# Kernel optimization log

Measured on AMD Instinct MI355X. Metric: run time of the kernel, lower is better.

Reference implementation:

```python
import jax, jax.numpy as jnp
import numpy as np

K = 20           # neighbors
ALPHA = 1.0      # clustering alpha
BN_EPS = 1e-5
NEG_SLOPE = 0.2


def knn_idx(x, k):
    # x: (B, C, N) -> idx (B, N, k) of k nearest neighbors by squared L2
    xx = jnp.sum(x * x, axis=1)                      # (B, N)
    inner = jnp.einsum('bcn,bcm->bnm', x, x)         # (B, N, N)
    pd = -xx[:, :, None] + 2.0 * inner - xx[:, None, :]  # negative sq dist
    return jax.lax.top_k(pd, k)[1]


def graph_feature(x, k):
    # x: (B, C, N) -> (B, 2C, N, k): concat(neighbor - center, center)
    xt = jnp.transpose(x, (0, 2, 1))                 # (B, N, C)
    idx = knn_idx(x, k)                              # (B, N, k)
    feat = jax.vmap(lambda f, i: f[i])(xt, idx)      # (B, N, k, C)
    center = jnp.broadcast_to(xt[:, :, None, :], feat.shape)
    out = jnp.concatenate([feat - center, center], axis=-1)
    return jnp.transpose(out, (0, 3, 1, 2))


def batchnorm(x, g, b, axes):
    # training-mode BN: batch statistics over `axes`, channel axis = 1
    m = jnp.mean(x, axes, keepdims=True)
    v = jnp.var(x, axes, keepdims=True)
    shape = [1] * x.ndim
    shape[1] = x.shape[1]
    return (x - m) / jnp.sqrt(v + BN_EPS) * g.reshape(shape) + b.reshape(shape)


def conv_block2d(x, w, g, b):
    # 1x1 Conv2d (no bias) + BN2d + LeakyReLU; x (B,Cin,N,k), w (Cout,Cin)
    y = jnp.einsum('oc,bcnk->bonk', w, x)
    return jax.nn.leaky_relu(batchnorm(y, g, b, (0, 2, 3)), NEG_SLOPE)


def setup_inputs() -> dict:
    key = jax.random.key(0)
    ks = jax.random.split(key, 16)
    B, C, N = 4, 3, 2048
    d = {
        'x1': jax.random.normal(ks[0], (B, C, N), jnp.float32),
        'x2': jax.random.normal(ks[1], (B, C, N), jnp.float32),
        'w1': jax.random.normal(ks[2], (64, 6), jnp.float32) * 0.1,
        'g1': jnp.ones((64,), jnp.float32), 'b1': jnp.zeros((64,), jnp.float32),
        'w2': jax.random.normal(ks[3], (64, 128), jnp.float32) * 0.1,
        'g2': jnp.ones((64,), jnp.float32), 'b2': jnp.zeros((64,), jnp.float32),
        'w3': jax.random.normal(ks[4], (128, 128), jnp.float32) * 0.1,
        'g3': jnp.ones((128,), jnp.float32), 'b3': jnp.zeros((128,), jnp.float32),
        'w4': jax.random.normal(ks[5], (256, 256), jnp.float32) * 0.1,
        'g4': jnp.ones((256,), jnp.float32), 'b4': jnp.zeros((256,), jnp.float32),
        'w5': jax.random.normal(ks[6], (1024, 512), jnp.float32) * 0.05,
        'g5': jnp.ones((1024,), jnp.float32), 'b5': jnp.zeros((1024,), jnp.float32),
        'lw1': jax.random.normal(ks[7], (256, 2048), jnp.float32) * 0.02,
        'lb1': jnp.zeros((256,), jnp.float32),
        'lw2': jax.random.normal(ks[8], (64, 256), jnp.float32) * 0.05,
        'lb2': jnp.zeros((64,), jnp.float32),
        'lw3': jax.random.normal(ks[9], (10, 64), jnp.float32) * 0.1,
        'lb3': jnp.zeros((10,), jnp.float32),
        'cw': jax.random.normal(ks[10], (800, 10), jnp.float32) * 0.1,
    }
    return d


def reference(x1, x2, w1, g1, b1, w2, g2, b2, w3, g3, b3, w4, g4, b4,
              w5, g5, b5, lw1, lb1, lw2, lb2, lw3, lb3, cw):

    def single(x):
        h = conv_block2d(graph_feature(x, K), w1, g1, b1)
        f1 = h.max(axis=-1)                            # (B,64,N)
        h = conv_block2d(graph_feature(f1, K), w2, g2, b2)
        f2 = h.max(axis=-1)                            # (B,64,N)
        h = conv_block2d(graph_feature(f2, K), w3, g3, b3)
        f3 = h.max(axis=-1)                            # (B,128,N)
        h = conv_block2d(graph_feature(f3, K), w4, g4, b4)
        f4 = h.max(axis=-1)                            # (B,256,N)
        h = jnp.concatenate([f1, f2, f3, f4], axis=1)  # (B,512,N)
        h = jnp.einsum('oc,bcn->bon', w5, h)           # 1x1 Conv1d
        h = jax.nn.leaky_relu(batchnorm(h, g5, b5, (0, 2)), NEG_SLOPE)
        z = jnp.concatenate([h.max(axis=-1), h.mean(axis=-1)], axis=1)  # (B,2048)
        z = z @ lw1.T + lb1
        z = z @ lw2.T + lb2
        e = z @ lw3.T + lb3                            # (B,10)
        diff = e[:, None, :] - cw                      # (B,800,10)
        x_dis = jnp.sum(diff * diff, axis=2)           # (B,800)
        q = (1.0 + x_dis / ALPHA) ** (-(ALPHA + 1.0) / 2.0)
        q = q / jnp.sum(q, axis=1, keepdims=True)
        return q, e, x_dis

    q1, e1, xd1 = single(x1)
    q2, e2, xd2 = single(x2)
    d = e1 - e2 + 1e-6  # torch F.pairwise_distance eps
    sim = jnp.sqrt(jnp.sum(d * d, axis=1))
    return (sim, q1, q2, e1, e2, xd1)
```

## Files before the change

kernel.cpp:

```cpp
#include <hip/hip_runtime.h>
#include <math.h>

#define BB 4
#define NN 2048
#define KK 20
#define NEG 0.2f

#define QOFF0 4
#define QOFF1 3204
#define EOFF0 6404
#define EOFF1 6444
#define XDOFF 6484

typedef unsigned short u16;
typedef unsigned int u32;
typedef __attribute__((ext_vector_type(8))) short s16x8;
typedef __attribute__((ext_vector_type(16))) float f32x16;
typedef __attribute__((ext_vector_type(8))) u16 u16x8;

__global__ __launch_bounds__(256) void transpose_x_kernel(
    const float* __restrict__ x, float* __restrict__ fnc, float* __restrict__ xx)
{
    int gid = blockIdx.x * 256 + threadIdx.x;
    int b = gid >> 11, n = gid & 2047;
    float s = 0.f;
#pragma unroll
    for (int c = 0; c < 3; ++c) {
        float v = x[((size_t)b * 3 + c) * NN + n];
        fnc[(size_t)gid * 3 + c] = v;
        s += v * v;
    }
    xx[gid] = s;
}

__global__ __launch_bounds__(256) void norms_kernel(
    const float* __restrict__ h512, int choff, int C, float* __restrict__ xx)
{
    int gid = blockIdx.x * 256 + threadIdx.x;
    const float* p = h512 + (size_t)gid * 512 + choff;
    float s = 0.f;
    for (int c = 0; c < C; ++c) { float v = p[c]; s += v * v; }
    xx[gid] = s;
}

template<int CTRL>
__device__ __forceinline__ float dmax(float v)
{
    int vi = __float_as_int(v);
    int nv = __builtin_amdgcn_update_dpp(vi, vi, CTRL, 0xf, 0xf, false);
    return fmaxf(v, __int_as_float(nv));
}

template<int C>
__global__ __launch_bounds__(512, 4) void knn_kernel(
    const float* __restrict__ fcn,
    const float* __restrict__ fnc,
    int ncs, int choff,
    const float* __restrict__ xx, int* __restrict__ idxout)
{
    __shared__ float sbuf[8][NN];
    int tid = threadIdx.x;
    int bid = blockIdx.x;
    int b   = bid & 3;
    int n0  = (((bid >> 3) << 1) | ((bid >> 2) & 1)) * 8;

    const float* fb = fcn + (size_t)b * C * NN;
    const float* xb = xx + b * NN;
    const float* cbase = fnc + (size_t)(b * NN + n0) * ncs + choff;

    float a0[8], a1[8], a2[8], a3[8];
#pragma unroll
    for (int r = 0; r < 8; ++r) { a0[r] = 0.f; a1[r] = 0.f; a2[r] = 0.f; a3[r] = 0.f; }

    const float* fp = fb + 4 * tid;

    if constexpr (C % 4 == 0) {
        float4 buf[4];
#pragma unroll
        for (int q = 0; q < 4; ++q) buf[q] = *(const float4*)(fp + (size_t)q * NN);
        for (int cg = 0; cg < C; cg += 4) {
            float4 nxt[4];
            if (cg + 4 < C) {
#pragma unroll
                for (int q = 0; q < 4; ++q)
                    nxt[q] = *(const float4*)(fp + (size_t)(cg + 4 + q) * NN);
            } else {
#pragma unroll
                for (int q = 0; q < 4; ++q) nxt[q] = buf[q];
            }
            float4 cv[8];
#pragma unroll
            for (int r = 0; r < 8; ++r)
                cv[r] = *(const float4*)(cbase + (size_t)r * ncs + cg);
#pragma unroll
            for (int r = 0; r < 8; ++r) {
                a0[r] += cv[r].x * buf[0].x; a1[r] += cv[r].x * buf[0].y;
                a2[r] += cv[r].x * buf[0].z; a3[r] += cv[r].x * buf[0].w;
                a0[r] += cv[r].y * buf[1].x; a1[r] += cv[r].y * buf[1].y;
                a2[r] += cv[r].y * buf[1].z; a3[r] += cv[r].y * buf[1].w;
                a0[r] += cv[r].z * buf[2].x; a1[r] += cv[r].z * buf[2].y;
                a2[r] += cv[r].z * buf[2].z; a3[r] += cv[r].z * buf[2].w;
                a0[r] += cv[r].w * buf[3].x; a1[r] += cv[r].w * buf[3].y;
                a2[r] += cv[r].w * buf[3].z; a3[r] += cv[r].w * buf[3].w;
            }
#pragma unroll
            for (int q = 0; q < 4; ++q) buf[q] = nxt[q];
        }
    } else {
        for (int c = 0; c < C; ++c) {
            float cr[8];
#pragma unroll
            for (int r = 0; r < 8; ++r) cr[r] = cbase[(size_t)r * ncs + c];
            float4 v = *(const float4*)(fp + (size_t)c * NN);
#pragma unroll
            for (int r = 0; r < 8; ++r) {
                a0[r] += cr[r] * v.x; a1[r] += cr[r] * v.y;
                a2[r] += cr[r] * v.z; a3[r] += cr[r] * v.w;
            }
        }
    }
    {
        float4 xm = *(const float4*)(xb + 4 * tid);
#pragma unroll
        for (int r = 0; r < 8; ++r) {
            float4 sv = {2.f * a0[r] - xm.x, 2.f * a1[r] - xm.y,
                         2.f * a2[r] - xm.z, 2.f * a3[r] - xm.w};
            *(float4*)&sbuf[r][4 * tid] = sv;
        }
    }
    __syncthreads();

    int w = tid >> 6, lane = tid & 63;
    float* sb = sbuf[w];
    int p = n0 + w;
    int* op = idxout + (size_t)(b * NN + p) * KK;
    const float NINF = -3.4e38f;

    float rv[32];
#pragma unroll
    for (int j = 0; j < 32; ++j) {
        float vv = sb[lane + (j << 6)];
        rv[j] = (lane + (j << 6) == p) ? NINF : vv;
    }
    if (lane == 0) op[0] = p;

    unsigned consumed = 0u;

    float v1 = NINF, v2 = NINF; int j1 = -1, j2 = -1;
#pragma unroll
    for (int j = 0; j < 32; ++j) {
        float vv = rv[j];
        if (vv > v1) { v2 = v1; j2 = j1; v1 = vv; j1 = j; }
        else if (vv > v2) { v2 = vv; j2 = j; }
    }
    int i1 = (j1 < 0) ? -1 : lane + (j1 << 6);
    int i2 = (j2 < 0) ? -1 : lane + (j2 << 6);

    for (int it = 1; it < KK; ++it) {
        float bv = v1;
        bv = dmax<0x111>(bv);
        bv = dmax<0x112>(bv);
        bv = dmax<0x114>(bv);
        bv = dmax<0x118>(bv);
        bv = dmax<0x142>(bv);
        bv = dmax<0x143>(bv);
        float smax = __int_as_float(
            __builtin_amdgcn_readlane(__float_as_int(bv), 63));
        unsigned long long mm = __ballot(v1 == smax);
        int owner = __ffsll(mm) - 1;
        if (lane == owner) {
            op[it] = i1;
            consumed |= 1u << j1;
            v1 = v2; i1 = i2; j1 = j2;
            v2 = NINF; i2 = -1; j2 = -1;
        }
        if (__any(v1 == NINF)) {
            if (v1 == NINF) {
                v1 = NINF; v2 = NINF; j1 = -1; j2 = -1;
#pragma unroll
                for (int j = 0; j < 32; ++j) {
                    if (!(consumed & (1u << j))) {
                        float vv = rv[j];
                        if (vv > v1) { v2 = v1; j2 = j1; v1 = vv; j1 = j; }
                        else if (vv > v2) { v2 = vv; j2 = j; }
                    }
                }
                i1 = (j1 < 0) ? -1 : lane + (j1 << 6);
                i2 = (j2 < 0) ? -1 : lane + (j2 << 6);
            }
        }
    }
}

template<int C, int COUT>
__global__ __launch_bounds__(256) void gemm_gh_kernel(
    const float* __restrict__ fnc, int ncs, int choff,
    const float* __restrict__ W,
    float* __restrict__ G, float* __restrict__ H)
{
    constexpr int GROUPS = 256 / COUT;
    constexpr int RPT = 8 / GROUPS;
    __shared__ float Fs[8][C];
    int tid = threadIdx.x;
    int row0 = blockIdx.x * 8;
    for (int i = tid; i < 8 * C; i += 256) {
        int r = i / C, c = i % C;
        Fs[r][c] = fnc[(size_t)(row0 + r) * ncs + choff + c];
    }
    __syncthreads();
    int o = tid % COUT;
    int r0 = (tid / COUT) * RPT;
    float g[RPT], h[RPT];
#pragma unroll
    for (int r = 0; r < RPT; ++r) { g[r] = 0.f; h[r] = 0.f; }
    const float* wr = W + (size_t)o * 2 * C;
    for (int c = 0; c < C; ++c) {
        float w1 = wr[c], wd = wr[C + c] - w1;
#pragma unroll
        for (int r = 0; r < RPT; ++r) {
            float f = Fs[r0 + r][c];
            g[r] += f * w1; h[r] += f * wd;
        }
    }
#pragma unroll
    for (int r = 0; r < RPT; ++r) {
        size_t rr = (size_t)(row0 + r0 + r) * COUT + o;
        G[rr] = g[r]; H[rr] = h[r];
    }
}

template<int COUT>
__global__ __launch_bounds__(256) void gather_kernel(
    const float* __restrict__ G, const float* __restrict__ H,
    const int* __restrict__ idx,
    float* __restrict__ ymax, float* __restrict__ ymin,
    float* __restrict__ psum, float* __restrict__ psumsq)
{
    constexpr int RPI = 256 / COUT;
    constexpr int NITER = 16 / RPI;
    int tid = threadIdx.x;
    int o = tid % COUT;
    int rsub = tid / COUT;
    int row0 = blockIdx.x * 16;
    float s = 0.f, s2 = 0.f;
    for (int it = 0; it < NITER; ++it) {
        int r = row0 + it * RPI + rsub;
        int b = r >> 11;
        float h = H[(size_t)r * COUT + o];
        const int* ip = idx + (size_t)r * KK;
        float mx = -3.4e38f, mn = 3.4e38f;
#pragma unroll
        for (int j = 0; j < KK; ++j) {
            int m = ip[j];
            float g = G[((size_t)(b << 11) + m) * COUT + o];
            float y = g + h;
            mx = fmaxf(mx, y); mn = fminf(mn, y);
            s += y; s2 += y * y;
        }
        ymax[(size_t)r * COUT + o] = mx;
        ymin[(size_t)r * COUT + o] = mn;
    }
    __shared__ float ls[256], ls2[256];
    ls[tid] = s; ls2[tid] = s2;
    __syncthreads();
    for (int st = 128; st >= COUT; st >>= 1) {
        if (tid < st) { ls[tid] += ls[tid + st]; ls2[tid] += ls2[tid + st]; }
        __syncthreads();
    }
    if (tid < COUT) {
        psum[(size_t)blockIdx.x * COUT + tid]   = ls[tid];
        psumsq[(size_t)blockIdx.x * COUT + tid] = ls2[tid];
    }
}

__global__ __launch_bounds__(256) void bnscale_kernel(
    const float* __restrict__ psum, const float* __restrict__ psumsq,
    int nblk, int cout, float cnt,
    const float* __restrict__ gw, const float* __restrict__ bw,
    float* __restrict__ ss)
{
    int o = blockIdx.x;
    int t = threadIdx.x;
    float s = 0.f, s2 = 0.f;
    for (int i = t; i < nblk; i += 256) {
        s  += psum[(size_t)i * cout + o];
        s2 += psumsq[(size_t)i * cout + o];
    }
    __shared__ float ls[256], ls2[256];
    ls[t] = s; ls2[t] = s2;
    __syncthreads();
    for (int st = 128; st > 0; st >>= 1) {
        if (t < st) { ls[t] += ls[t + st]; ls2[t] += ls2[t + st]; }
        __syncthreads();
    }
    if (t == 0) {
        float m = ls[0] / cnt;
        float v = ls2[0] / cnt - m * m;
        float sc = gw[o] / sqrtf(v + 1e-5f);
        float sh = bw[o] - m * sc;
        ss[o * 2] = sc; ss[o * 2 + 1] = sh;
    }
}

__global__ __launch_bounds__(256) void apply_kernel(
    const float* __restrict__ ymax, const float* __restrict__ ymin,
    const float* __restrict__ ss, int coutShift, int choff,
    float* __restrict__ h512)
{
    size_t gid = (size_t)blockIdx.x * 256 + threadIdx.x;
    int o = (int)(gid & ((1u << coutShift) - 1));
    size_t r = gid >> coutShift;
    float sc = ss[o * 2], sh = ss[o * 2 + 1];
    float v = (sc >= 0.f) ? ymax[gid] : ymin[gid];
    float a = sc * v + sh;
    float act = (a > 0.f) ? a : NEG * a;
    h512[r * 512 + choff + o] = act;
}

template<int CO>
__global__ __launch_bounds__(256) void apply_t_kernel(
    const float* __restrict__ ymax, const float* __restrict__ ymin,
    const float* __restrict__ ss, int choff,
    float* __restrict__ h512, float* __restrict__ fcn)
{
    constexpr int TILES_O = CO >> 6;
    __shared__ float tile[64][65];
    int tr = blockIdx.x / TILES_O;
    int to = blockIdx.x % TILES_O;
    int r0 = tr * 64, o0 = to * 64;
    int t = threadIdx.x;
    int lr = t >> 6;
    int lo = t & 63;
    int o = o0 + lo;
    float sc = ss[o * 2], sh = ss[o * 2 + 1];
#pragma unroll
    for (int rr = 0; rr < 64; rr += 4) {
        int r = r0 + rr + lr;
        size_t gid = (size_t)r * CO + o;
        float v = (sc >= 0.f) ? ymax[gid] : ymin[gid];
        float a = sc * v + sh;
        float act = (a > 0.f) ? a : NEG * a;
        h512[(size_t)r * 512 + choff + o] = act;
        tile[rr + lr][lo] = act;
    }
    __syncthreads();
    int b = r0 >> 11;
    int n0 = r0 & 2047;
#pragma unroll
    for (int oo = 0; oo < 64; oo += 4) {
        fcn[((size_t)(b * CO + o0 + oo + lr)) * NN + n0 + lo] = tile[lo][oo + lr];
    }
}

__device__ __forceinline__ u16 f2bf(float x) {
    u32 u = __float_as_uint(x);
    u += 0x7FFFu + ((u >> 16) & 1u);
    return (u16)(u >> 16);
}

__global__ __launch_bounds__(256) void tobf16_kernel(
    const float* __restrict__ A, const float* __restrict__ Bm,
    u16* __restrict__ Ah, u16* __restrict__ Al,
    u16* __restrict__ Bh, u16* __restrict__ Bl)
{
    int gid = blockIdx.x * 256 + threadIdx.x;
    const float* src; u16 *dh, *dl; size_t off;
    if (gid < 524288) { src = A;  dh = Ah; dl = Al; off = (size_t)gid * 8; }
    else             { src = Bm; dh = Bh; dl = Bl; off = (size_t)(gid - 524288) * 8; }
    float4 v0 = *(const float4*)(src + off);
    float4 v1 = *(const float4*)(src + off + 4);
    float x[8] = {v0.x, v0.y, v0.z, v0.w, v1.x, v1.y, v1.z, v1.w};
    u16x8 h, l;
#pragma unroll
    for (int j = 0; j < 8; ++j) {
        u16 hb = f2bf(x[j]);
        h[j] = hb;
        l[j] = f2bf(x[j] - __uint_as_float((u32)hb << 16));
    }
    *(u16x8*)(dh + off) = h;
    *(u16x8*)(dl + off) = l;
}

__device__ __forceinline__ void gload_lds16(const void* g, void* l) {
    __builtin_amdgcn_global_load_lds(
        (const __attribute__((address_space(1))) void*)g,
        (__attribute__((address_space(3))) void*)l, 16, 0, 0);
}

__global__ __launch_bounds__(256) void gemm5_mfma_kernel(
    const u16* __restrict__ Ah, const u16* __restrict__ Al,
    const u16* __restrict__ Bh, const u16* __restrict__ Bl,
    float* __restrict__ Y, float* __restrict__ psum, float* __restrict__ psumsq)
{
    __shared__ u16 As[2][128][64];
    __shared__ u16 Bs[2][128][64];
    __shared__ float scs[4][128];
    __shared__ float sqs[4][128];

    int tid = threadIdx.x;
    int bm = blockIdx.x & 63, bn = blockIdx.x >> 6;
    int row0 = bm * 128, col0 = bn * 128;
    int w = tid >> 6, lane = tid & 63;
    int wr = w >> 1, wc = w & 1;

    int isB = w >> 1, plane = w & 1;
    int srow = lane >> 3;
    int kch  = (lane & 7) ^ srow;
    const u16* gbase = isB ? (plane ? Bl : Bh) : (plane ? Al : Ah);
    int rc0 = isB ? col0 : row0;
    const u16* gsrc0 = gbase + (size_t)(rc0 + srow) * 512 + kch * 8;
    u16* lds0 = (isB ? &Bs[0][0][0] : &As[0][0][0]) + plane * 8192;

    f32x16 acc[2][2];
#pragma unroll
    for (int i = 0; i < 2; ++i)
#pragma unroll
        for (int j = 0; j < 2; ++j)
#pragma unroll
            for (int r = 0; r < 16; ++r) acc[i][j][r] = 0.f;

    int ln = lane & 31, l5 = lane >> 5;
    const u16* Afb = &As[0][0][0] + (size_t)(wr * 64 + ln) * 64;
    const u16* Bfb = &Bs[0][0][0] + (size_t)(wc * 64 + ln) * 64;

    for (int k0 = 0; k0 < 512; k0 += 64) {
#pragma unroll
        for (int cc = 0; cc < 16; ++cc)
            gload_lds16(gsrc0 + (size_t)cc * 4096 + k0, lds0 + cc * 512);
        __syncthreads();

#pragma unroll
        for (int ks = 0; ks < 4; ++ks) {
            int pos = ((ks * 2 + l5) ^ (ln & 7)) * 8;
            s16x8 ah0 = *(const s16x8*)(Afb + pos);
            s16x8 ah1 = *(const s16x8*)(Afb + 2048 + pos);
            s16x8 al0 = *(const s16x8*)(Afb + 8192 + pos);
            s16x8 al1 = *(const s16x8*)(Afb + 8192 + 2048 + pos);
#pragma unroll
            for (int j = 0; j < 2; ++j) {
                s16x8 bh = *(const s16x8*)(Bfb + j * 2048 + pos);
                s16x8 bl = *(const s16x8*)(Bfb + 8192 + j * 2048 + pos);
                acc[0][j] = __builtin_amdgcn_mfma_f32_32x32x16_bf16(ah0, bh, acc[0][j], 0, 0, 0);
                acc[1][j] = __builtin_amdgcn_mfma_f32_32x32x16_bf16(ah1, bh, acc[1][j], 0, 0, 0);
                acc[0][j] = __builtin_amdgcn_mfma_f32_32x32x16_bf16(al0, bh, acc[0][j], 0, 0, 0);
                acc[1][j] = __builtin_amdgcn_mfma_f32_32x32x16_bf16(al1, bh, acc[1][j], 0, 0, 0);
                acc[0][j] = __builtin_amdgcn_mfma_f32_32x32x16_bf16(ah0, bl, acc[0][j], 0, 0, 0);
                acc[1][j] = __builtin_amdgcn_mfma_f32_32x32x16_bf16(ah1, bl, acc[1][j], 0, 0, 0);
            }
        }
        __syncthreads();
    }

#pragma unroll
    for (int i = 0; i < 2; ++i)
#pragma unroll
        for (int reg = 0; reg < 16; ++reg) {
            int row = row0 + wr * 64 + i * 32 + l5 * 4 + (reg >> 2) * 8 + (reg & 3);
            float* yp = Y + (size_t)row * 1024 + col0 + wc * 64 + ln;
            yp[0]  = acc[i][0][reg];
            yp[32] = acc[i][1][reg];
        }

#pragma unroll
    for (int j = 0; j < 2; ++j) {
        float s = 0.f, q = 0.f;
#pragma unroll
        for (int i = 0; i < 2; ++i)
#pragma unroll
            for (int reg = 0; reg < 16; ++reg) {
                float v = acc[i][j][reg];
                s += v; q += v * v;
            }
        scs[wr * 2 + l5][wc * 64 + j * 32 + ln] = s;
        sqs[wr * 2 + l5][wc * 64 + j * 32 + ln] = q;
    }
    __syncthreads();
    if (tid < 128) {
        float s = 0.f, q = 0.f;
#pragma unroll
        for (int p = 0; p < 4; ++p) { s += scs[p][tid]; q += sqs[p][tid]; }
        psum[(size_t)bm * 1024 + col0 + tid]   = s;
        psumsq[(size_t)bm * 1024 + col0 + tid] = q;
    }
}

__global__ __launch_bounds__(256) void pool_part_kernel(
    const float* __restrict__ Y, const float* __restrict__ ss,
    float* __restrict__ pmax, float* __restrict__ psum)
{
    int bid = blockIdx.x;
    int b = bid >> 6;
    int n0 = (bid & 63) * 32;
    int t = threadIdx.x;
    int o = t * 4;
    float4 sA = *(const float4*)(ss + o * 2);
    float4 sB = *(const float4*)(ss + o * 2 + 4);
    float4 mx = {-3.4e38f, -3.4e38f, -3.4e38f, -3.4e38f};
    float4 sm = {0.f, 0.f, 0.f, 0.f};
    const float* Yb = Y + ((size_t)b * NN + n0) * 1024 + o;
#pragma unroll 4
    for (int n = 0; n < 32; ++n) {
        float4 v = *(const float4*)(Yb + (size_t)n * 1024);
        float a0 = sA.x * v.x + sA.y; a0 = (a0 > 0.f) ? a0 : NEG * a0;
        float a1 = sA.z * v.y + sA.w; a1 = (a1 > 0.f) ? a1 : NEG * a1;
        float a2 = sB.x * v.z + sB.y; a2 = (a2 > 0.f) ? a2 : NEG * a2;
        float a3 = sB.z * v.w + sB.w; a3 = (a3 > 0.f) ? a3 : NEG * a3;
        mx.x = fmaxf(mx.x, a0); sm.x += a0;
        mx.y = fmaxf(mx.y, a1); sm.y += a1;
        mx.z = fmaxf(mx.z, a2); sm.z += a2;
        mx.w = fmaxf(mx.w, a3); sm.w += a3;
    }
    size_t po = (size_t)bid * 1024 + o;
    *(float4*)(pmax + po) = mx;
    *(float4*)(psum + po) = sm;
}

__global__ __launch_bounds__(256) void pool_comb_kernel(
    const float* __restrict__ pmax, const float* __restrict__ psum,
    float* __restrict__ z)
{
    int b = blockIdx.x;
    int t = threadIdx.x;
    int o = t * 4;
    float4 mx = {-3.4e38f, -3.4e38f, -3.4e38f, -3.4e38f};
    float4 sm = {0.f, 0.f, 0.f, 0.f};
    for (int ch = 0; ch < 64; ++ch) {
        size_t po = ((size_t)(b * 64 + ch)) * 1024 + o;
        float4 m = *(const float4*)(pmax + po);
        float4 s = *(const float4*)(psum + po);
        mx.x = fmaxf(mx.x, m.x); mx.y = fmaxf(mx.y, m.y);
        mx.z = fmaxf(mx.z, m.z); mx.w = fmaxf(mx.w, m.w);
        sm.x += s.x; sm.y += s.y; sm.z += s.z; sm.w += s.w;
    }
    *(float4*)(z + (size_t)b * 2048 + o) = mx;
    float4 mn = {sm.x * (1.f / 2048.f), sm.y * (1.f / 2048.f),
                 sm.z * (1.f / 2048.f), sm.w * (1.f / 2048.f)};
    *(float4*)(z + (size_t)b * 2048 + 1024 + o) = mn;
}

__global__ __launch_bounds__(64) void gemv1_kernel(
    const float* __restrict__ z, const float* __restrict__ lw1,
    const float* __restrict__ lb1, float* __restrict__ z1)
{
    int o = blockIdx.x;
    int lane = threadIdx.x;
    const float* wr = lw1 + (size_t)o * 2048;
    float a0 = 0.f, a1 = 0.f, a2 = 0.f, a3 = 0.f;
    for (int c = lane; c < 2048; c += 64) {
        float w = wr[c];
        a0 += z[c] * w; a1 += z[2048 + c] * w;
        a2 += z[4096 + c] * w; a3 += z[6144 + c] * w;
    }
#pragma unroll
    for (int off = 32; off > 0; off >>= 1) {
        a0 += __shfl_down(a0, off); a1 += __shfl_down(a1, off);
        a2 += __shfl_down(a2, off); a3 += __shfl_down(a3, off);
    }
    if (lane == 0) {
        float bias = lb1[o];
        z1[o] = a0 + bias; z1[256 + o] = a1 + bias;
        z1[512 + o] = a2 + bias; z1[768 + o] = a3 + bias;
    }
}

__global__ __launch_bounds__(1024) void head2_kernel(
    const float* __restrict__ z1,
    const float* __restrict__ lw2, const float* __restrict__ lb2,
    const float* __restrict__ lw3, const float* __restrict__ lb3,
    const float* __restrict__ cw,
    float* __restrict__ out, float* __restrict__ e_store, int which)
{
    __shared__ float z2s[4][64];
    __shared__ float es[4][10];
    __shared__ float qs[3200];
    __shared__ float dnm[4];
    int t = threadIdx.x;
    if (t < 256) {
        int b = t >> 6, o = t & 63;
        float acc = lb2[o];
        const float* wr = lw2 + (size_t)o * 256;
        const float* zr = z1 + b * 256;
        for (int c = 0; c < 256; ++c) acc += zr[c] * wr[c];
        z2s[b][o] = acc;
    }
    __syncthreads();
    if (t < 40) {
        int b = t / 10, o = t % 10;
        float acc = lb3[o];
        const float* wr = lw3 + o * 64;
        for (int c = 0; c < 64; ++c) acc += z2s[b][c] * wr[c];
        es[b][o] = acc;
        int eoff = (which == 0) ? EOFF0 : EOFF1;
        out[eoff + b * 10 + o] = acc;
        e_store[which * 40 + b * 10 + o] = acc;
    }
    __syncthreads();
    for (int p = t; p < 3200; p += 1024) {
        int b = p / 800, j = p % 800;
        float xd = 0.f;
        const float* cwr = cw + j * 10;
#pragma unroll
        for (int i = 0; i < 10; ++i) { float d = es[b][i] - cwr[i]; xd += d * d; }
        qs[p] = 1.0f / (1.0f + xd);
        if (which == 0) out[XDOFF + p] = xd;
    }
    __syncthreads();
    if (t < 4) {
        float s = 0.f;
        for (int j = 0; j < 800; ++j) s += qs[t * 800 + j];
        dnm[t] = s;
    }
    __syncthreads();
    int qoff = (which == 0) ? QOFF0 : QOFF1;
    for (int p = t; p < 3200; p += 1024) out[qoff + p] = qs[p] / dnm[p / 800];
}

__global__ void sim_kernel(const float* __restrict__ e_store, float* __restrict__ out)
{
    int t = threadIdx.x;
    if (t < 4) {
        float s = 0.f;
        for (int i = 0; i < 10; ++i) {
            float d = e_store[t * 10 + i] - e_store[40 + t * 10 + i] + 1e-6f;
            s += d * d;
        }
        out[t] = sqrtf(s);
    }
}

extern "C" void kernel_launch(void* const* d_in, const int* in_sizes, int n_in,
                              void* d_out, int out_size, void* d_ws, size_t ws_size,
                              hipStream_t stream)
{
    const float* x1  = (const float*)d_in[0];
    const float* x2  = (const float*)d_in[1];
    const float* w1  = (const float*)d_in[2];
    const float* g1  = (const float*)d_in[3];
    const float* b1  = (const float*)d_in[4];
    const float* w2  = (const float*)d_in[5];
    const float* g2  = (const float*)d_in[6];
    const float* b2  = (const float*)d_in[7];
    const float* w3  = (const float*)d_in[8];
    const float* g3  = (const float*)d_in[9];
    const float* b3  = (const float*)d_in[10];
    const float* w4  = (const float*)d_in[11];
    const float* g4  = (const float*)d_in[12];
    const float* b4  = (const float*)d_in[13];
    const float* w5  = (const float*)d_in[14];
    const float* g5  = (const float*)d_in[15];
    const float* b5  = (const float*)d_in[16];
    const float* lw1 = (const float*)d_in[17];
    const float* lb1 = (const float*)d_in[18];
    const float* lw2 = (const float*)d_in[19];
    const float* lb2 = (const float*)d_in[20];
    const float* lw3 = (const float*)d_in[21];
    const float* lb3 = (const float*)d_in[22];
    const float* cw  = (const float*)d_in[23];
    float* out = (float*)d_out;

    float* ws   = (float*)d_ws;
    float* h512 = ws;
    float* G    = h512 + 4194304;
    float* Hb   = G + 2097152;
    float* ymax = Hb + 2097152;
    float* ymin = ymax + 2097152;
    float* y5   = G;
    float* fcn  = ymin + 2097152;
    float* fnc1 = fcn + 1048576;
    float* xx   = fnc1 + 32768;
    float* psum = xx + 8192;
    float* psq  = psum + 131072;
    float* ss   = psq + 131072;
    float* p5s  = ss + 2048;
    float* p5q  = p5s + 262144;
    float* ss5  = p5q + 262144;
    float* z    = ss5 + 2048;
    float* z1   = z + 8192;
    float* est  = z1 + 1024;
    int*   idx  = (int*)(est + 128);
    u16*   Ahs  = (u16*)(idx + BB * NN * KK);
    u16*   Als  = Ahs + 4194304;
    u16*   Bhs  = Als + 4194304;
    u16*   Bls  = Bhs + 524288;

    for (int which = 0; which < 2; ++which) {
        const float* xin = which ? x2 : x1;
        transpose_x_kernel<<<32, 256, 0, stream>>>(xin, fnc1, xx);
        knn_kernel<3><<<1024, 512, 0, stream>>>(xin, fnc1, 3, 0, xx, idx);
        gemm_gh_kernel<3, 64><<<1024, 256, 0, stream>>>(fnc1, 3, 0, w1, G, Hb);
        gather_kernel<64><<<512, 256, 0, stream>>>(G, Hb, idx, ymax, ymin, psum, psq);
        bnscale_kernel<<<64, 256, 0, stream>>>(psum, psq, 512, 64, 163840.f, g1, b1, ss);
        apply_t_kernel<64><<<128, 256, 0, stream>>>(ymax, ymin, ss, 0, h512, fcn);
        norms_kernel<<<32, 256, 0, stream>>>(h512, 0, 64, xx);
        knn_kernel<64><<<1024, 512, 0, stream>>>(fcn, h512, 512, 0, xx, idx);
        gemm_gh_kernel<64, 64><<<1024, 256, 0, stream>>>(h512, 512, 0, w2, G, Hb);
        gather_kernel<64><<<512, 256, 0, stream>>>(G, Hb, idx, ymax, ymin, psum, psq);
        bnscale_kernel<<<64, 256, 0, stream>>>(psum, psq, 512, 64, 163840.f, g2, b2, ss);
        apply_t_kernel<64><<<128, 256, 0, stream>>>(ymax, ymin, ss, 64, h512, fcn);
        norms_kernel<<<32, 256, 0, stream>>>(h512, 64, 64, xx);
        knn_kernel<64><<<1024, 512, 0, stream>>>(fcn, h512, 512, 64, xx, idx);
        gemm_gh_kernel<64, 128><<<1024, 256, 0, stream>>>(h512, 512, 64, w3, G, Hb);
        gather_kernel<128><<<512, 256, 0, stream>>>(G, Hb, idx, ymax, ymin, psum, psq);
        bnscale_kernel<<<128, 256, 0, stream>>>(psum, psq, 512, 128, 163840.f, g3, b3, ss);
        apply_t_kernel<128><<<256, 256, 0, stream>>>(ymax, ymin, ss, 128, h512, fcn);
        norms_kernel<<<32, 256, 0, stream>>>(h512, 128, 128, xx);
        knn_kernel<128><<<1024, 512, 0, stream>>>(fcn, h512, 512, 128, xx, idx);
        gemm_gh_kernel<128, 256><<<1024, 256, 0, stream>>>(h512, 512, 128, w4, G, Hb);
        gather_kernel<256><<<512, 256, 0, stream>>>(G, Hb, idx, ymax, ymin, psum, psq);
        bnscale_kernel<<<256, 256, 0, stream>>>(psum, psq, 512, 256, 163840.f, g4, b4, ss);
        apply_kernel<<<8192, 256, 0, stream>>>(ymax, ymin, ss, 8, 256, h512);
        tobf16_kernel<<<2304, 256, 0, stream>>>(h512, w5, Ahs, Als, Bhs, Bls);
        gemm5_mfma_kernel<<<512, 256, 0, stream>>>(Ahs, Als, Bhs, Bls, y5, p5s, p5q);
        bnscale_kernel<<<1024, 256, 0, stream>>>(p5s, p5q, 64, 1024, 8192.f, g5, b5, ss5);
        pool_part_kernel<<<256, 256, 0, stream>>>(y5, ss5, p5s, p5q);
        pool_comb_kernel<<<4, 256, 0, stream>>>(p5s, p5q, z);
        gemv1_kernel<<<256, 64, 0, stream>>>(z, lw1, lb1, z1);
        head2_kernel<<<1, 1024, 0, stream>>>(z1, lw2, lb2, lw3, lb3, cw, out, est, which);
    }
    sim_kernel<<<1, 64, 0, stream>>>(est, out);
}
```

Baseline: 1.226 ms.

## Process two query rows per wave in kNN and keep top-3 candidates per lane

The kNN kernel now handles 16 query points per block in two dot-product passes, so each wave runs two independent top-k selections whose DPP reductions and ballots are interleaved for instruction-level parallelism. Each lane tracks a top-3 instead of a top-2 list to make costly rescans of its 32 register values less frequent. The grid is halved to match. In exchange, register pressure roughly doubles (two 32-float arrays plus state), which could cause spills or reduce occupancy under the 512x4 launch bounds, and there is an extra shared-memory round trip with additional syncs.

```diff
diff --git a/kernel.cpp b/kernel.cpp
--- a/kernel.cpp
+++ b/kernel.cpp
@@ -51,28 +51,16 @@
     return fmaxf(v, __int_as_float(nv));
 }
 
+#define NINFV -3.4e38f
+
 template<int C>
-__global__ __launch_bounds__(512, 4) void knn_kernel(
-    const float* __restrict__ fcn,
-    const float* __restrict__ fnc,
-    int ncs, int choff,
-    const float* __restrict__ xx, int* __restrict__ idxout)
-{
-    __shared__ float sbuf[8][NN];
-    int tid = threadIdx.x;
-    int bid = blockIdx.x;
-    int b   = bid & 3;
-    int n0  = (((bid >> 3) << 1) | ((bid >> 2) & 1)) * 8;
-
-    const float* fb = fcn + (size_t)b * C * NN;
-    const float* xb = xx + b * NN;
-    const float* cbase = fnc + (size_t)(b * NN + n0) * ncs + choff;
-
+__device__ __forceinline__ void dot_phase(
+    const float* __restrict__ fp, const float* __restrict__ cbase, int ncs,
+    float4 xm, float (*sbuf)[NN], int tid)
+{
     float a0[8], a1[8], a2[8], a3[8];
 #pragma unroll
     for (int r = 0; r < 8; ++r) { a0[r] = 0.f; a1[r] = 0.f; a2[r] = 0.f; a3[r] = 0.f; }
-
-    const float* fp = fb + 4 * tid;
 
     if constexpr (C % 4 == 0) {
         float4 buf[4];
@@ -119,75 +107,120 @@
             }
         }
     }
-    {
-        float4 xm = *(const float4*)(xb + 4 * tid);
-#pragma unroll
-        for (int r = 0; r < 8; ++r) {
-            float4 sv = {2.f * a0[r] - xm.x, 2.f * a1[r] - xm.y,
-                         2.f * a2[r] - xm.z, 2.f * a3[r] - xm.w};
-            *(float4*)&sbuf[r][4 * tid] = sv;
-        }
-    }
-    __syncthreads();
-
-    int w = tid >> 6, lane = tid & 63;
-    float* sb = sbuf[w];
-    int p = n0 + w;
-    int* op = idxout + (size_t)(b * NN + p) * KK;
-    const float NINF = -3.4e38f;
-
-    float rv[32];
-#pragma unroll
-    for (int j = 0; j < 32; ++j) {
-        float vv = sb[lane + (j << 6)];
-        rv[j] = (lane + (j << 6) == p) ? NINF : vv;
-    }
-    if (lane == 0) op[0] = p;
-
-    unsigned consumed = 0u;
-
-    float v1 = NINF, v2 = NINF; int j1 = -1, j2 = -1;
+#pragma unroll
+    for (int r = 0; r < 8; ++r) {
+        float4 sv = {2.f * a0[r] - xm.x, 2.f * a1[r] - xm.y,
+                     2.f * a2[r] - xm.z, 2.f * a3[r] - xm.w};
+        *(float4*)&sbuf[r][4 * tid] = sv;
+    }
+}
+
+__device__ __forceinline__ void top3_init(const float (&rv)[32],
+    float& v1, float& v2, float& v3, int& j1, int& j2, int& j3)
+{
+    v1 = NINFV; v2 = NINFV; v3 = NINFV; j1 = -1; j2 = -1; j3 = -1;
 #pragma unroll
     for (int j = 0; j < 32; ++j) {
         float vv = rv[j];
-        if (vv > v1) { v2 = v1; j2 = j1; v1 = vv; j1 = j; }
-        else if (vv > v2) { v2 = vv; j2 = j; }
-    }
-    int i1 = (j1 < 0) ? -1 : lane + (j1 << 6);
-    int i2 = (j2 < 0) ? -1 : lane + (j2 << 6);
+        if (vv > v1) { v3 = v2; j3 = j2; v2 = v1; j2 = j1; v1 = vv; j1 = j; }
+        else if (vv > v2) { v3 = v2; j3 = j2; v2 = vv; j2 = j; }
+        else if (vv > v3) { v3 = vv; j3 = j; }
+    }
+}
+
+__device__ __forceinline__ void top3_rebuild(const float (&rv)[32], unsigned c,
+    float& v1, float& v2, float& v3, int& j1, int& j2, int& j3)
+{
+    v1 = NINFV; v2 = NINFV; v3 = NINFV; j1 = -1; j2 = -1; j3 = -1;
+#pragma unroll
+    for (int j = 0; j < 32; ++j) {
+        if (!(c & (1u << j))) {
+            float vv = rv[j];
+            if (vv > v1) { v3 = v2; j3 = j2; v2 = v1; j2 = j1; v1 = vv; j1 = j; }
+            else if (vv > v2) { v3 = v2; j3 = j2; v2 = vv; j2 = j; }
+            else if (vv > v3) { v3 = vv; j3 = j; }
+        }
+    }
+}
+
+template<int C>
+__global__ __launch_bounds__(512, 4) void knn_kernel(
+    const float* __restrict__ fcn,
+    const float* __restrict__ fnc,
+    int ncs, int choff,
+    const float* __restrict__ xx, int* __restrict__ idxout)
+{
+    __shared__ float sbuf[8][NN];
+    int tid = threadIdx.x;
+    int bid = blockIdx.x;
+    int b   = bid & 3;
+    int n0  = (bid >> 2) * 16;
+
+    const float* fb = fcn + (size_t)b * C * NN;
+    const float* xb = xx + b * NN;
+    const float* fp = fb + 4 * tid;
+    float4 xm = *(const float4*)(xb + 4 * tid);
+
+    int w = tid >> 6, lane = tid & 63;
+    int pA = n0 + w, pB = n0 + 8 + w;
+
+    float rvA[32], rvB[32];
+
+    dot_phase<C>(fp, fnc + (size_t)(b * NN + n0) * ncs + choff, ncs, xm, sbuf, tid);
+    __syncthreads();
+#pragma unroll
+    for (int j = 0; j < 32; ++j) {
+        float vv = sbuf[w][lane + (j << 6)];
+        rvA[j] = (lane + (j << 6) == pA) ? NINFV : vv;
+    }
+    __syncthreads();
+    dot_phase<C>(fp, fnc + (size_t)(b * NN + n0 + 8) * ncs + choff, ncs, xm, sbuf, tid);
+    __syncthreads();
+#pragma unroll
+    for (int j = 0; j < 32; ++j) {
+        float vv = sbuf[w][lane + (j << 6)];
+        rvB[j] = (lane + (j << 6) == pB) ? NINFV : vv;
+    }
+
+    int* opA = idxout + (size_t)(b * NN + pA) * KK;
+    int* opB = idxout + (size_t)(b * NN + pB) * KK;
+    if (lane == 0) { opA[0] = pA; opB[0] = pB; }
+
+    unsigned cA = 0u, cB = 0u;
+    float v1A, v2A, v3A, v1B, v2B, v3B;
+    int j1A, j2A, j3A, j1B, j2B, j3B;
+    top3_init(rvA, v1A, v2A, v3A, j1A, j2A, j3A);
+    top3_init(rvB, v1B, v2B, v3B, j1B, j2B, j3B);
 
     for (int it = 1; it < KK; ++it) {
-        float bv = v1;
-        bv = dmax<0x111>(bv);
-        bv = dmax<0x112>(bv);
-        bv = dmax<0x114>(bv);
-        bv = dmax<0x118>(bv);
-        bv = dmax<0x142>(bv);
-        bv = dmax<0x143>(bv);
-        float smax = __int_as_float(
-            __builtin_amdgcn_readlane(__float_as_int(bv), 63));
-        unsigned long long mm = __ballot(v1 == smax);
-        int owner = __ffsll(mm) - 1;
-        if (lane == owner) {
-            op[it] = i1;
-            consumed |= 1u << j1;
-            v1 = v2; i1 = i2; j1 = j2;
-            v2 = NINF; i2 = -1; j2 = -1;
-        }
-        if (__any(v1 == NINF)) {
-            if (v1 == NINF) {
-                v1 = NINF; v2 = NINF; j1 = -1; j2 = -1;
-#pragma unroll
-                for (int j = 0; j < 32; ++j) {
-                    if (!(consumed & (1u << j))) {
-                        float vv = rv[j];
-                        if (vv > v1) { v2 = v1; j2 = j1; v1 = vv; j1 = j; }
-                        else if (vv > v2) { v2 = vv; j2 = j; }
-                    }
-                }
-                i1 = (j1 < 0) ? -1 : lane + (j1 << 6);
-                i2 = (j2 < 0) ? -1 : lane + (j2 << 6);
-            }
+        float bvA = v1A, bvB = v1B;
+        bvA = dmax<0x111>(bvA); bvB = dmax<0x111>(bvB);
+        bvA = dmax<0x112>(bvA); bvB = dmax<0x112>(bvB);
+        bvA = dmax<0x114>(bvA); bvB = dmax<0x114>(bvB);
+        bvA = dmax<0x118>(bvA); bvB = dmax<0x118>(bvB);
+        bvA = dmax<0x142>(bvA); bvB = dmax<0x142>(bvB);
+        bvA = dmax<0x143>(bvA); bvB = dmax<0x143>(bvB);
+        float smA = __int_as_float(
+            __builtin_amdgcn_readlane(__float_as_int(bvA), 63));
+        float smB = __int_as_float(
+            __builtin_amdgcn_readlane(__float_as_int(bvB), 63));
+        unsigned long long mA = __ballot(v1A == smA);
+        unsigned long long mB = __ballot(v1B == smB);
+        if (lane == __ffsll(mA) - 1) {
+            opA[it] = lane + (j1A << 6);
+            cA |= 1u << j1A;
+            v1A = v2A; j1A = j2A; v2A = v3A; j2A = j3A; v3A = NINFV; j3A = -1;
+        }
+        if (lane == __ffsll(mB) - 1) {
+            opB[it] = lane + (j1B << 6);
+            cB |= 1u << j1B;
+            v1B = v2B; j1B = j2B; v2B = v3B; j2B = j3B; v3B = NINFV; j3B = -1;
+        }
+        if (__any(v1A == NINFV)) {
+            if (v1A == NINFV) top3_rebuild(rvA, cA, v1A, v2A, v3A, j1A, j2A, j3A);
+        }
+        if (__any(v1B == NINFV)) {
+            if (v1B == NINFV) top3_rebuild(rvB, cB, v1B, v2B, v3B, j1B, j2B, j3B);
         }
     }
 }
@@ -686,25 +719,25 @@
     for (int which = 0; which < 2; ++which) {
         const float* xin = which ? x2 : x1;
         transpose_x_kernel<<<32, 256, 0, stream>>>(xin, fnc1, xx);
-        knn_kernel<3><<<1024, 512, 0, stream>>>(xin, fnc1, 3, 0, xx, idx);
+        knn_kernel<3><<<512, 512, 0, stream>>>(xin, fnc1, 3, 0, xx, idx);
         gemm_gh_kernel<3, 64><<<1024, 256, 0, stream>>>(fnc1, 3, 0, w1, G, Hb);
         gather_kernel<64><<<512, 256, 0, stream>>>(G, Hb, idx, ymax, ymin, psum, psq);
         bnscale_kernel<<<64, 256, 0, stream>>>(psum, psq, 512, 64, 163840.f, g1, b1, ss);
         apply_t_kernel<64><<<128, 256, 0, stream>>>(ymax, ymin, ss, 0, h512, fcn);
         norms_kernel<<<32, 256, 0, stream>>>(h512, 0, 64, xx);
-        knn_kernel<64><<<1024, 512, 0, stream>>>(fcn, h512, 512, 0, xx, idx);
+        knn_kernel<64><<<512, 512, 0, stream>>>(fcn, h512, 512, 0, xx, idx);
         gemm_gh_kernel<64, 64><<<1024, 256, 0, stream>>>(h512, 512, 0, w2, G, Hb);
         gather_kernel<64><<<512, 256, 0, stream>>>(G, Hb, idx, ymax, ymin, psum, psq);
         bnscale_kernel<<<64, 256, 0, stream>>>(psum, psq, 512, 64, 163840.f, g2, b2, ss);
         apply_t_kernel<64><<<128, 256, 0, stream>>>(ymax, ymin, ss, 64, h512, fcn);
         norms_kernel<<<32, 256, 0, stream>>>(h512, 64, 64, xx);
-        knn_kernel<64><<<1024, 512, 0, stream>>>(fcn, h512, 512, 64, xx, idx);
+        knn_kernel<64><<<512, 512, 0, stream>>>(fcn, h512, 512, 64, xx, idx);
         gemm_gh_kernel<64, 128><<<1024, 256, 0, stream>>>(h512, 512, 64, w3, G, Hb);
         gather_kernel<128><<<512, 256, 0, stream>>>(G, Hb, idx, ymax, ymin, psum, psq);
         bnscale_kernel<<<128, 256, 0, stream>>>(psum, psq, 512, 128, 163840.f, g3, b3, ss);
         apply_t_kernel<128><<<256, 256, 0, stream>>>(ymax, ymin, ss, 128, h512, fcn);
         norms_kernel<<<32, 256, 0, stream>>>(h512, 128, 128, xx);
-        knn_kernel<128><<<1024, 512, 0, stream>>>(fcn, h512, 512, 128, xx, idx);
+        knn_kernel<128><<<512, 512, 0, stream>>>(fcn, h512, 512, 128, xx, idx);
         gemm_gh_kernel<128, 256><<<1024, 256, 0, stream>>>(h512, 512, 128, w4, G, Hb);
         gather_kernel<256><<<512, 256, 0, stream>>>(G, Hb, idx, ymax, ymin, psum, psq);
         bnscale_kernel<<<256, 256, 0, stream>>>(psum, psq, 512, 256, 163840.f, g4, b4, ss);
```

Result: slower. 1.874 ms (+52.9%).

## Extract two top-k winners per wave reduction using per-lane top-4 lists

Applied to the files above, without the earlier changes.

The kNN selection now keeps a sorted top-4 candidate list per lane instead of top-2, and each DPP reduction tracks the wave's top two values at once. Two neighbor indices are emitted per reduction round, roughly halving the serial reduction steps across the 19 selections. The register array of distances is dropped and rescans read from shared memory instead, which lowers register pressure but adds LDS loads whenever a lane runs low on candidates. The top-4 insertion adds branchy compare work, and ties between equal values may be handled differently from before.

```diff
diff --git a/kernel.cpp b/kernel.cpp
--- a/kernel.cpp
+++ b/kernel.cpp
@@ -43,12 +43,19 @@
     xx[gid] = s;
 }
 
+#define NINFV -3.4e38f
+
 template<int CTRL>
-__device__ __forceinline__ float dmax(float v)
-{
-    int vi = __float_as_int(v);
-    int nv = __builtin_amdgcn_update_dpp(vi, vi, CTRL, 0xf, 0xf, false);
-    return fmaxf(v, __int_as_float(nv));
+__device__ __forceinline__ void dmax2(float& a1, float& a2)
+{
+    int b1i = __builtin_amdgcn_update_dpp(
+        __float_as_int(a1), __float_as_int(a1), CTRL, 0xf, 0xf, false);
+    int b2i = __builtin_amdgcn_update_dpp(
+        __float_as_int(a2), __float_as_int(a2), CTRL, 0xf, 0xf, false);
+    float b1 = __int_as_float(b1i), b2 = __int_as_float(b2i);
+    float n1 = fmaxf(a1, b1);
+    float n2 = fmaxf(fminf(a1, b1), fmaxf(a2, b2));
+    a1 = n1; a2 = n2;
 }
 
 template<int C>
@@ -134,59 +141,65 @@
     float* sb = sbuf[w];
     int p = n0 + w;
     int* op = idxout + (size_t)(b * NN + p) * KK;
-    const float NINF = -3.4e38f;
-
-    float rv[32];
+
+    if (lane == 0) op[0] = p;
+    if (lane == (p & 63)) sb[p] = NINFV;
+
+    float v1 = NINFV, v2 = NINFV, v3 = NINFV, v4 = NINFV;
+    int j1 = -1, j2 = -1, j3 = -1, j4 = -1;
 #pragma unroll
     for (int j = 0; j < 32; ++j) {
         float vv = sb[lane + (j << 6)];
-        rv[j] = (lane + (j << 6) == p) ? NINF : vv;
-    }
-    if (lane == 0) op[0] = p;
+        if (vv > v1) { v4 = v3; j4 = j3; v3 = v2; j3 = j2; v2 = v1; j2 = j1; v1 = vv; j1 = j; }
+        else if (vv > v2) { v4 = v3; j4 = j3; v3 = v2; j3 = j2; v2 = vv; j2 = j; }
+        else if (vv > v3) { v4 = v3; j4 = j3; v3 = vv; j3 = j; }
+        else if (vv > v4) { v4 = vv; j4 = j; }
+    }
 
     unsigned consumed = 0u;
 
-    float v1 = NINF, v2 = NINF; int j1 = -1, j2 = -1;
-#pragma unroll
-    for (int j = 0; j < 32; ++j) {
-        float vv = rv[j];
-        if (vv > v1) { v2 = v1; j2 = j1; v1 = vv; j1 = j; }
-        else if (vv > v2) { v2 = vv; j2 = j; }
-    }
-    int i1 = (j1 < 0) ? -1 : lane + (j1 << 6);
-    int i2 = (j2 < 0) ? -1 : lane + (j2 << 6);
-
-    for (int it = 1; it < KK; ++it) {
-        float bv = v1;
-        bv = dmax<0x111>(bv);
-        bv = dmax<0x112>(bv);
-        bv = dmax<0x114>(bv);
-        bv = dmax<0x118>(bv);
-        bv = dmax<0x142>(bv);
-        bv = dmax<0x143>(bv);
-        float smax = __int_as_float(
-            __builtin_amdgcn_readlane(__float_as_int(bv), 63));
-        unsigned long long mm = __ballot(v1 == smax);
-        int owner = __ffsll(mm) - 1;
-        if (lane == owner) {
-            op[it] = i1;
+    for (int it = 1; it < KK; it += 2) {
+        float r1 = v1, r2 = v2;
+        dmax2<0x111>(r1, r2);
+        dmax2<0x112>(r1, r2);
+        dmax2<0x114>(r1, r2);
+        dmax2<0x118>(r1, r2);
+        dmax2<0x142>(r1, r2);
+        dmax2<0x143>(r1, r2);
+        float m1 = __int_as_float(
+            __builtin_amdgcn_readlane(__float_as_int(r1), 63));
+        float m2 = __int_as_float(
+            __builtin_amdgcn_readlane(__float_as_int(r2), 63));
+        unsigned long long k1 = __ballot(v1 == m1);
+        if (lane == __ffsll(k1) - 1) {
+            op[it] = lane + (j1 << 6);
             consumed |= 1u << j1;
-            v1 = v2; i1 = i2; j1 = j2;
-            v2 = NINF; i2 = -1; j2 = -1;
-        }
-        if (__any(v1 == NINF)) {
-            if (v1 == NINF) {
-                v1 = NINF; v2 = NINF; j1 = -1; j2 = -1;
+            v1 = v2; j1 = j2; v2 = v3; j2 = j3; v3 = v4; j3 = j4;
+            v4 = NINFV; j4 = -1;
+        }
+        if (it + 1 < KK) {
+            unsigned long long k2 = __ballot(v1 == m2);
+            if (lane == __ffsll(k2) - 1) {
+                op[it + 1] = lane + (j1 << 6);
+                consumed |= 1u << j1;
+                v1 = v2; j1 = j2; v2 = v3; j2 = j3; v3 = v4; j3 = j4;
+                v4 = NINFV; j4 = -1;
+            }
+        }
+        if (__any(v2 == NINFV)) {
+            if (v2 == NINFV) {
+                v1 = NINFV; v2 = NINFV; v3 = NINFV; v4 = NINFV;
+                j1 = -1; j2 = -1; j3 = -1; j4 = -1;
 #pragma unroll
                 for (int j = 0; j < 32; ++j) {
                     if (!(consumed & (1u << j))) {
-                        float vv = rv[j];
-                        if (vv > v1) { v2 = v1; j2 = j1; v1 = vv; j1 = j; }
-                        else if (vv > v2) { v2 = vv; j2 = j; }
+                        float vv = sb[lane + (j << 6)];
+                        if (vv > v1) { v4 = v3; j4 = j3; v3 = v2; j3 = j2; v2 = v1; j2 = j1; v1 = vv; j1 = j; }
+                        else if (vv > v2) { v4 = v3; j4 = j3; v3 = v2; j3 = j2; v2 = vv; j2 = j; }
+                        else if (vv > v3) { v4 = v3; j4 = j3; v3 = vv; j3 = j; }
+                        else if (vv > v4) { v4 = vv; j4 = j; }
                     }
                 }
-                i1 = (j1 < 0) ? -1 : lane + (j1 << 6);
-                i2 = (j2 < 0) ? -1 : lane + (j2 << 6);
             }
         }
     }
```

Result: faster. 1.170 ms (-4.5%).
